# Kernel optimization log

Hardware: AMD Instinct MI355X
Metric: run time of the kernel (lower is better)

The kernel has to match this reference:

```python
import jax, jax.numpy as jnp
import numpy as np

NUM_HEADS = 32
NUM_KV_HEADS = 8
HEAD_DIM = 128
WINDOW = 256
NUM_META = 128
ROPE_BASE = 10000.0


def _rope_cos_sin(seq_len, dim, dtype):
    inv_freq = 1.0 / (ROPE_BASE ** (jnp.arange(0, dim, 2, dtype=jnp.float32) / dim))
    pos = jnp.arange(seq_len, dtype=jnp.float32)
    freqs = pos[:, None] * inv_freq[None, :]          # [S, dim/2]
    emb = jnp.concatenate([freqs, freqs], axis=-1)     # [S, dim]
    return emb.astype(dtype) * 0 + jnp.cos(emb).astype(dtype), jnp.sin(emb).astype(dtype)


def _rotate_half(x):
    x1, x2 = jnp.split(x, 2, axis=-1)
    return jnp.concatenate([-x2, x1], axis=-1)


def setup_inputs() -> dict:
    key = jax.random.key(0)
    k1, k2, k3 = jax.random.split(key, 3)
    B, S = 1, 2176
    return {
        "query_states": jax.random.normal(k1, (B, S, NUM_HEADS * HEAD_DIM), dtype=jnp.float32),
        "key_states": jax.random.normal(k2, (B, S, NUM_KV_HEADS * HEAD_DIM), dtype=jnp.float32),
        "value_states": jax.random.normal(k3, (B, S, NUM_KV_HEADS * HEAD_DIM), dtype=jnp.float32),
    }


def reference(query_states, key_states, value_states):
    B, S, _ = query_states.shape
    n_rep = NUM_HEADS // NUM_KV_HEADS

    q = query_states.reshape(B, S, NUM_HEADS, HEAD_DIM).transpose(0, 2, 1, 3)      # [B,H,S,D]
    k = key_states.reshape(B, S, NUM_KV_HEADS, HEAD_DIM).transpose(0, 2, 1, 3)     # [B,Hk,S,D]
    v = value_states.reshape(B, S, NUM_KV_HEADS, HEAD_DIM).transpose(0, 2, 1, 3)

    # GQA expansion: repeat_interleave along head dim
    k = jnp.repeat(k, n_rep, axis=1)   # [B,H,S,D]
    v = jnp.repeat(v, n_rep, axis=1)

    # inline RoPE on q and (expanded) k
    cos, sin = _rope_cos_sin(S, HEAD_DIM, q.dtype)     # [S,D]
    cos = cos[None, None]
    sin = sin[None, None]
    q = q * cos + _rotate_half(q) * sin
    k = k * cos + _rotate_half(k) * sin

    scale = 1.0 / jnp.sqrt(jnp.asarray(HEAD_DIM, q.dtype))
    scores = jnp.einsum("bhqd,bhkd->bhqk", q, k) * scale

    # mask: causal AND (sliding window OR kv is a prefix meta token)
    q_idx = jnp.arange(S)[:, None]
    kv_idx = jnp.arange(S)[None, :]
    causal = q_idx >= kv_idx
    sliding = (q_idx - kv_idx) <= WINDOW
    prefix = kv_idx < NUM_META
    mask = causal & (sliding | prefix)                 # [S,S]

    scores = jnp.where(mask[None, None], scores, jnp.asarray(-jnp.inf, scores.dtype))
    probs = jax.nn.softmax(scores, axis=-1)
    out = jnp.einsum("bhqk,bhkd->bhqd", probs, v)      # [B,H,S,D]
    return out.transpose(0, 2, 1, 3).reshape(B, S, NUM_HEADS * HEAD_DIM)
```

## Files before the change

kernel.cpp:

```cpp
#include <hip/hip_runtime.h>

#define HQ 32
#define HKV 8
#define DH 128
#define WIN 256
#define META 128
#define QSCALE 0.1275174324f
#define NFREQ 0.20762050594046f

typedef __attribute__((ext_vector_type(8))) __bf16 bf16x8;
typedef __attribute__((ext_vector_type(16))) float f32x16;
typedef __attribute__((ext_vector_type(4))) unsigned int u32x4;
typedef unsigned short u16;
typedef unsigned int u32;

__device__ __forceinline__ u16 f2bf(float f) {
  u32 u = __float_as_uint(f);
  u += 0x7FFFu + ((u >> 16) & 1u);
  return (u16)(u >> 16);
}
__device__ __forceinline__ u32 packbf(float a, float b) {
  u32 ua = __float_as_uint(a); ua += 0x7FFFu + ((ua >> 16) & 1u);
  u32 ub = __float_as_uint(b); ub += 0x7FFFu + ((ub >> 16) & 1u);
  return (ua >> 16) | (ub & 0xFFFF0000u);
}

__global__ __launch_bounds__(256)
void prep_kv(const float* __restrict__ Kg, const float* __restrict__ Vg,
             u16* __restrict__ Kr, u16* __restrict__ Vt, int S) {
  __shared__ float T[64][132];
  const int hk = blockIdx.x;
  const int s0 = blockIdx.y * 64;
  const int tid = threadIdx.x;
  {
    const int r = tid >> 2, c0 = (tid & 3) * 16;
    const int s = s0 + r;
    const float pos = (float)s;
    const float* src = Kg + ((size_t)s * HKV + hk) * DH;
    u16* dst = Kr + ((size_t)hk * S + s) * DH;
    float x[16], y[16];
    #pragma unroll
    for (int j = 0; j < 16; j += 4) {
      *(float4*)&x[j] = *(const float4*)(src + c0 + j);
      *(float4*)&y[j] = *(const float4*)(src + c0 + 64 + j);
    }
    u16 lo[16], hb[16];
    #pragma unroll
    for (int j = 0; j < 16; ++j) {
      float iv = __builtin_amdgcn_exp2f(-NFREQ * (float)(c0 + j));
      float sv, cv; __sincosf(pos * iv, &sv, &cv);
      lo[j] = f2bf(x[j] * cv - y[j] * sv);
      hb[j] = f2bf(y[j] * cv + x[j] * sv);
    }
    *(int4*)(dst + c0)      = *(int4*)&lo[0];
    *(int4*)(dst + c0 + 8)  = *(int4*)&lo[8];
    *(int4*)(dst + c0 + 64) = *(int4*)&hb[0];
    *(int4*)(dst + c0 + 72) = *(int4*)&hb[8];
  }
  {
    const int r = tid >> 2, c = (tid & 3) * 32;
    const float* src = Vg + ((size_t)(s0 + r) * HKV + hk) * DH + c;
    #pragma unroll
    for (int j = 0; j < 32; j += 4) *(float4*)&T[r][c + j] = *(const float4*)(src + j);
  }
  __syncthreads();
  {
    const int d = tid >> 1, hf = (tid & 1) * 32;
    u16 buf[32];
    #pragma unroll
    for (int i = 0; i < 32; ++i) buf[i] = f2bf(T[hf + i][d]);
    u16* dst = Vt + ((size_t)hk * DH + d) * S + s0 + hf;
    #pragma unroll
    for (int j = 0; j < 4; ++j) *(int4*)(dst + j * 8) = *(int4*)&buf[j * 8];
  }
}

__global__ __launch_bounds__(256, 2)
void attn_main(const float* __restrict__ Qg, const u16* __restrict__ Kr,
               const u16* __restrict__ Vt, float* __restrict__ Og, int S) {
  const int h = blockIdx.x;
  const int nqb = gridDim.y;
  const int q0 = (nqb - 1 - blockIdx.y) * 128;
  const int hk = h >> 2;
  const int tid = threadIdx.x;
  const int lane = tid & 63;
  const int wave = tid >> 6;
  const int ln31 = lane & 31;
  const int hi = lane >> 5;
  const int kh = hi * 8;

  __shared__ __align__(16) char smem[35840];
  u16 (*Qs)[136] = (u16(*)[136])smem;
  u16 (*Ks)[136] = (u16(*)[136])smem;
  u16 (*Vs)[72]  = (u16(*)[72])(smem + 17408);

  {
    const int r = tid >> 1, c0 = (tid & 1) * 32;
    const float pos = (float)(q0 + r);
    const float* qrow = Qg + ((size_t)(q0 + r) * HQ + h) * DH;
    #pragma unroll
    for (int c = c0; c < c0 + 32; c += 8) {
      float x[8], y[8];
      *(float4*)&x[0] = *(const float4*)(qrow + c);
      *(float4*)&x[4] = *(const float4*)(qrow + c + 4);
      *(float4*)&y[0] = *(const float4*)(qrow + c + 64);
      *(float4*)&y[4] = *(const float4*)(qrow + c + 68);
      u16 lo[8], hb[8];
      #pragma unroll
      for (int j = 0; j < 8; ++j) {
        float iv = __builtin_amdgcn_exp2f(-NFREQ * (float)(c + j));
        float sv, cv; __sincosf(pos * iv, &sv, &cv);
        lo[j] = f2bf((x[j] * cv - y[j] * sv) * QSCALE);
        hb[j] = f2bf((y[j] * cv + x[j] * sv) * QSCALE);
      }
      __builtin_memcpy(&Qs[r][c], lo, 16);
      __builtin_memcpy(&Qs[r][c + 64], hb, 16);
    }
  }
  __syncthreads();
  const int qw0 = q0 + wave * 32;
  const int q = qw0 + ln31;
  bf16x8 qa[8];
  {
    const u16* qb = &Qs[wave * 32 + ln31][kh];
    #pragma unroll
    for (int kk = 0; kk < 8; ++kk) qa[kk] = *(const bf16x8*)(qb + kk * 16);
  }

  int wstart = q0 - WIN; if (wstart < META) wstart = META;
  int nwin = (q0 + 128 - wstart) >> 6; if (nwin < 0) nwin = 0;
  const int ntiles = 2 + nwin;

  f32x16 acc[4];
  #pragma unroll
  for (int d = 0; d < 4; ++d)
    #pragma unroll
    for (int r = 0; r < 16; ++r) acc[d][r] = 0.f;
  float m_i = -1e30f, l_i = 0.f;

  const u16* Kb = Kr + (size_t)hk * S * DH;
  const u16* Vb = Vt + ((size_t)hk * DH + (tid >> 1)) * S + (tid & 1) * 32;
  const int kr = tid >> 2, kc = (tid & 3) * 32;

  for (int t = 0; t < ntiles; ++t) {
    const int kv0 = (t < 2) ? t * 64 : wstart + (t - 2) * 64;

    __syncthreads();
    {
      const int4* ks = (const int4*)(Kb + (size_t)(kv0 + kr) * DH + kc);
      int4 a = ks[0], b = ks[1], c = ks[2], d = ks[3];
      int4* kd = (int4*)&Ks[kr][kc];
      kd[0] = a; kd[1] = b; kd[2] = c; kd[3] = d;
    }
    {
      const int4* vs = (const int4*)(Vb + kv0);
      int4 a = vs[0], b = vs[1], c = vs[2], d = vs[3];
      int4* vd = (int4*)&Vs[tid >> 1][(tid & 1) * 32];
      vd[0] = a; vd[1] = b; vd[2] = c; vd[3] = d;
    }
    __syncthreads();

    const bool active = (kv0 <= qw0 + 31) &&
                        ((kv0 < META) || (qw0 - kv0 - 63 <= WIN));
    if (!active) continue;

    f32x16 s0v, s1v;
    #pragma unroll
    for (int r = 0; r < 16; ++r) { s0v[r] = 0.f; s1v[r] = 0.f; }
    const u16* ka0 = &Ks[ln31][kh];
    const u16* ka1 = &Ks[32 + ln31][kh];
    #pragma unroll
    for (int kk = 0; kk < 8; ++kk)
      s0v = __builtin_amdgcn_mfma_f32_32x32x16_bf16(*(const bf16x8*)(ka0 + kk * 16), qa[kk], s0v, 0, 0, 0);
    #pragma unroll
    for (int kk = 0; kk < 8; ++kk)
      s1v = __builtin_amdgcn_mfma_f32_32x32x16_bf16(*(const bf16x8*)(ka1 + kk * 16), qa[kk], s1v, 0, 0, 0);

    const bool fullv = (kv0 + 63 <= qw0) &&
                       ((kv0 + 63 < META) || (qw0 + 31 - kv0 <= WIN));
    if (!fullv) {
      #pragma unroll
      for (int r = 0; r < 16; ++r) {
        const int kva = kv0 + (r & 3) + 8 * (r >> 2) + 4 * hi;
        const int kvb = kva + 32;
        if (!((kva <= q) && (((q - kva) <= WIN) || (kva < META)))) s0v[r] = -1e30f;
        if (!((kvb <= q) && (((q - kvb) <= WIN) || (kvb < META)))) s1v[r] = -1e30f;
      }
    }

    float mx = -1e30f;
    #pragma unroll
    for (int r = 0; r < 16; ++r) mx = fmaxf(mx, fmaxf(s0v[r], s1v[r]));
    mx = fmaxf(mx, __shfl_xor(mx, 32));
    const float mnew = fmaxf(m_i, mx);
    const float al = __builtin_amdgcn_exp2f(m_i - mnew);
    m_i = mnew;
    float ps = 0.f;
    #pragma unroll
    for (int r = 0; r < 16; ++r) {
      s0v[r] = __builtin_amdgcn_exp2f(s0v[r] - mnew);
      s1v[r] = __builtin_amdgcn_exp2f(s1v[r] - mnew);
      ps += s0v[r] + s1v[r];
    }
    ps += __shfl_xor(ps, 32);
    l_i = l_i * al + ps;
    #pragma unroll
    for (int d = 0; d < 4; ++d)
      #pragma unroll
      for (int r = 0; r < 16; ++r) acc[d][r] *= al;

    u32 pk0[8], pk1[8], sh0[8], sh1[8];
    #pragma unroll
    for (int m = 0; m < 8; ++m) {
      pk0[m] = packbf(s0v[2 * m], s0v[2 * m + 1]);
      pk1[m] = packbf(s1v[2 * m], s1v[2 * m + 1]);
    }
    #pragma unroll
    for (int m = 0; m < 8; ++m) {
      sh0[m] = (u32)__shfl_xor((int)pk0[m], 32);
      sh1[m] = (u32)__shfl_xor((int)pk1[m], 32);
    }
    u32x4 bl0 = { hi ? sh0[2] : pk0[0], hi ? sh0[3] : pk0[1],
                  hi ? pk0[2] : sh0[0], hi ? pk0[3] : sh0[1] };
    u32x4 bh0 = { hi ? sh0[6] : pk0[4], hi ? sh0[7] : pk0[5],
                  hi ? pk0[6] : sh0[4], hi ? pk0[7] : sh0[5] };
    u32x4 bl1 = { hi ? sh1[2] : pk1[0], hi ? sh1[3] : pk1[1],
                  hi ? pk1[2] : sh1[0], hi ? pk1[3] : sh1[1] };
    u32x4 bh1 = { hi ? sh1[6] : pk1[4], hi ? sh1[7] : pk1[5],
                  hi ? pk1[6] : sh1[4], hi ? pk1[7] : sh1[5] };
    const bf16x8 pbl0 = __builtin_bit_cast(bf16x8, bl0);
    const bf16x8 pbh0 = __builtin_bit_cast(bf16x8, bh0);
    const bf16x8 pbl1 = __builtin_bit_cast(bf16x8, bl1);
    const bf16x8 pbh1 = __builtin_bit_cast(bf16x8, bh1);

    #pragma unroll
    for (int dt = 0; dt < 4; ++dt) {
      const u16* vrow = &Vs[dt * 32 + ln31][kh];
      acc[dt] = __builtin_amdgcn_mfma_f32_32x32x16_bf16(*(const bf16x8*)(vrow),      pbl0, acc[dt], 0, 0, 0);
      acc[dt] = __builtin_amdgcn_mfma_f32_32x32x16_bf16(*(const bf16x8*)(vrow + 16), pbh0, acc[dt], 0, 0, 0);
      acc[dt] = __builtin_amdgcn_mfma_f32_32x32x16_bf16(*(const bf16x8*)(vrow + 32), pbl1, acc[dt], 0, 0, 0);
      acc[dt] = __builtin_amdgcn_mfma_f32_32x32x16_bf16(*(const bf16x8*)(vrow + 48), pbh1, acc[dt], 0, 0, 0);
    }
  }

  const float inv = 1.0f / l_i;
  float* ob = Og + ((size_t)q * HQ + h) * DH;
  #pragma unroll
  for (int dt = 0; dt < 4; ++dt) {
    #pragma unroll
    for (int g = 0; g < 4; ++g) {
      float4 o = { acc[dt][4 * g + 0] * inv, acc[dt][4 * g + 1] * inv,
                   acc[dt][4 * g + 2] * inv, acc[dt][4 * g + 3] * inv };
      *(float4*)(ob + dt * 32 + 8 * g + 4 * hi) = o;
    }
  }
}

extern "C" void kernel_launch(void* const* d_in, const int* in_sizes, int n_in,
                              void* d_out, int out_size, void* d_ws, size_t ws_size,
                              hipStream_t stream) {
  const float* Qg = (const float*)d_in[0];
  const float* Kg = (const float*)d_in[1];
  const float* Vg = (const float*)d_in[2];
  float* Og = (float*)d_out;
  const int S = in_sizes[0] / (HQ * DH);

  u16* Kr = (u16*)d_ws;
  u16* Vt = (u16*)((char*)d_ws + (size_t)HKV * S * DH * 2);

  prep_kv<<<dim3(HKV, S / 64), dim3(256), 0, stream>>>(Kg, Vg, Kr, Vt, S);
  attn_main<<<dim3(HQ, S / 128), dim3(256), 0, stream>>>(Qg, Kr, Vt, Og, S);
}
```

Before: 136.3 us.

## Prefetch next K/V tile into registers while computing current tile

Global loads for the next K/V tile are issued into registers before the current tile's QK, softmax and PV work, and written to shared memory after it. The first tile's load is issued before the Q RoPE prologue. This is meant to hide global memory latency behind MFMA work. The cost is 32 more live VGPRs per thread under the 2-blocks-per-SM launch bound, which could cause spills or lower occupancy.

After: 133.3 us. 1.02x faster.

```diff
diff --git a/kernel.cpp b/kernel.cpp
--- a/kernel.cpp
+++ b/kernel.cpp
@@ -74,6 +74,20 @@
     for (int j = 0; j < 4; ++j) *(int4*)(dst + j * 8) = *(int4*)&buf[j * 8];
   }
 }
+
+#define LOAD_KV(kv0_) do {                                                 \
+    const int4* ks_ = (const int4*)(Kb + (size_t)((kv0_) + kr) * DH + kc); \
+    fk0 = ks_[0]; fk1 = ks_[1]; fk2 = ks_[2]; fk3 = ks_[3];                \
+    const int4* vs_ = (const int4*)(Vb + (kv0_));                          \
+    fv0 = vs_[0]; fv1 = vs_[1]; fv2 = vs_[2]; fv3 = vs_[3];                \
+  } while (0)
+
+#define STORE_KV() do {                                                    \
+    int4* kd_ = (int4*)&Ks[kr][kc];                                        \
+    kd_[0] = fk0; kd_[1] = fk1; kd_[2] = fk2; kd_[3] = fk3;                \
+    int4* vd_ = (int4*)&Vs[tid >> 1][(tid & 1) * 32];                      \
+    vd_[0] = fv0; vd_[1] = fv1; vd_[2] = fv2; vd_[3] = fv3;                \
+  } while (0)
 
 __global__ __launch_bounds__(256, 2)
 void attn_main(const float* __restrict__ Qg, const u16* __restrict__ Kr,
@@ -94,6 +108,13 @@
   u16 (*Ks)[136] = (u16(*)[136])smem;
   u16 (*Vs)[72]  = (u16(*)[72])(smem + 17408);
 
+  const u16* Kb = Kr + (size_t)hk * S * DH;
+  const u16* Vb = Vt + ((size_t)hk * DH + (tid >> 1)) * S + (tid & 1) * 32;
+  const int kr = tid >> 2, kc = (tid & 3) * 32;
+
+  int4 fk0, fk1, fk2, fk3, fv0, fv1, fv2, fv3;
+  LOAD_KV(0);
+
   {
     const int r = tid >> 1, c0 = (tid & 1) * 32;
     const float pos = (float)(q0 + r);
@@ -126,6 +147,9 @@
     #pragma unroll
     for (int kk = 0; kk < 8; ++kk) qa[kk] = *(const bf16x8*)(qb + kk * 16);
   }
+  __syncthreads();
+  STORE_KV();
+  __syncthreads();
 
   int wstart = q0 - WIN; if (wstart < META) wstart = META;
   int nwin = (q0 + 128 - wstart) >> 6; if (nwin < 0) nwin = 0;
@@ -138,108 +162,100 @@
     for (int r = 0; r < 16; ++r) acc[d][r] = 0.f;
   float m_i = -1e30f, l_i = 0.f;
 
-  const u16* Kb = Kr + (size_t)hk * S * DH;
-  const u16* Vb = Vt + ((size_t)hk * DH + (tid >> 1)) * S + (tid & 1) * 32;
-  const int kr = tid >> 2, kc = (tid & 3) * 32;
-
   for (int t = 0; t < ntiles; ++t) {
     const int kv0 = (t < 2) ? t * 64 : wstart + (t - 2) * 64;
-
-    __syncthreads();
-    {
-      const int4* ks = (const int4*)(Kb + (size_t)(kv0 + kr) * DH + kc);
-      int4 a = ks[0], b = ks[1], c = ks[2], d = ks[3];
-      int4* kd = (int4*)&Ks[kr][kc];
-      kd[0] = a; kd[1] = b; kd[2] = c; kd[3] = d;
-    }
-    {
-      const int4* vs = (const int4*)(Vb + kv0);
-      int4 a = vs[0], b = vs[1], c = vs[2], d = vs[3];
-      int4* vd = (int4*)&Vs[tid >> 1][(tid & 1) * 32];
-      vd[0] = a; vd[1] = b; vd[2] = c; vd[3] = d;
-    }
-    __syncthreads();
+    const bool haveNext = (t + 1 < ntiles);
+    if (haveNext) {
+      const int kvn = (t + 1 < 2) ? (t + 1) * 64 : wstart + (t - 1) * 64;
+      LOAD_KV(kvn);
+    }
 
     const bool active = (kv0 <= qw0 + 31) &&
                         ((kv0 < META) || (qw0 - kv0 - 63 <= WIN));
-    if (!active) continue;
-
-    f32x16 s0v, s1v;
-    #pragma unroll
-    for (int r = 0; r < 16; ++r) { s0v[r] = 0.f; s1v[r] = 0.f; }
-    const u16* ka0 = &Ks[ln31][kh];
-    const u16* ka1 = &Ks[32 + ln31][kh];
-    #pragma unroll
-    for (int kk = 0; kk < 8; ++kk)
-      s0v = __builtin_amdgcn_mfma_f32_32x32x16_bf16(*(const bf16x8*)(ka0 + kk * 16), qa[kk], s0v, 0, 0, 0);
-    #pragma unroll
-    for (int kk = 0; kk < 8; ++kk)
-      s1v = __builtin_amdgcn_mfma_f32_32x32x16_bf16(*(const bf16x8*)(ka1 + kk * 16), qa[kk], s1v, 0, 0, 0);
-
-    const bool fullv = (kv0 + 63 <= qw0) &&
-                       ((kv0 + 63 < META) || (qw0 + 31 - kv0 <= WIN));
-    if (!fullv) {
+    if (active) {
+      f32x16 s0v, s1v;
+      #pragma unroll
+      for (int r = 0; r < 16; ++r) { s0v[r] = 0.f; s1v[r] = 0.f; }
+      const u16* ka0 = &Ks[ln31][kh];
+      const u16* ka1 = &Ks[32 + ln31][kh];
+      #pragma unroll
+      for (int kk = 0; kk < 8; ++kk)
+        s0v = __builtin_amdgcn_mfma_f32_32x32x16_bf16(*(const bf16x8*)(ka0 + kk * 16), qa[kk], s0v, 0, 0, 0);
+      #pragma unroll
+      for (int kk = 0; kk < 8; ++kk)
+        s1v = __builtin_amdgcn_mfma_f32_32x32x16_bf16(*(const bf16x8*)(ka1 + kk * 16), qa[kk], s1v, 0, 0, 0);
+
+      const bool fullv = (kv0 + 63 <= qw0) &&
+                         ((kv0 + 63 < META) || (qw0 + 31 - kv0 <= WIN));
+      if (!fullv) {
+        #pragma unroll
+        for (int r = 0; r < 16; ++r) {
+          const int kva = kv0 + (r & 3) + 8 * (r >> 2) + 4 * hi;
+          const int kvb = kva + 32;
+          if (!((kva <= q) && (((q - kva) <= WIN) || (kva < META)))) s0v[r] = -1e30f;
+          if (!((kvb <= q) && (((q - kvb) <= WIN) || (kvb < META)))) s1v[r] = -1e30f;
+        }
+      }
+
+      float mx = -1e30f;
+      #pragma unroll
+      for (int r = 0; r < 16; ++r) mx = fmaxf(mx, fmaxf(s0v[r], s1v[r]));
+      mx = fmaxf(mx, __shfl_xor(mx, 32));
+      const float mnew = fmaxf(m_i, mx);
+      const float al = __builtin_amdgcn_exp2f(m_i - mnew);
+      m_i = mnew;
+      float ps = 0.f;
       #pragma unroll
       for (int r = 0; r < 16; ++r) {
-        const int kva = kv0 + (r & 3) + 8 * (r >> 2) + 4 * hi;
-        const int kvb = kva + 32;
-        if (!((kva <= q) && (((q - kva) <= WIN) || (kva < META)))) s0v[r] = -1e30f;
-        if (!((kvb <= q) && (((q - kvb) <= WIN) || (kvb < META)))) s1v[r] = -1e30f;
-      }
-    }
-
-    float mx = -1e30f;
-    #pragma unroll
-    for (int r = 0; r < 16; ++r) mx = fmaxf(mx, fmaxf(s0v[r], s1v[r]));
-    mx = fmaxf(mx, __shfl_xor(mx, 32));
-    const float mnew = fmaxf(m_i, mx);
-    const float al = __builtin_amdgcn_exp2f(m_i - mnew);
-    m_i = mnew;
-    float ps = 0.f;
-    #pragma unroll
-    for (int r = 0; r < 16; ++r) {
-      s0v[r] = __builtin_amdgcn_exp2f(s0v[r] - mnew);
-      s1v[r] = __builtin_amdgcn_exp2f(s1v[r] - mnew);
-      ps += s0v[r] + s1v[r];
-    }
-    ps += __shfl_xor(ps, 32);
-    l_i = l_i * al + ps;
-    #pragma unroll
-    for (int d = 0; d < 4; ++d)
-      #pragma unroll
-      for (int r = 0; r < 16; ++r) acc[d][r] *= al;
-
-    u32 pk0[8], pk1[8], sh0[8], sh1[8];
-    #pragma unroll
-    for (int m = 0; m < 8; ++m) {
-      pk0[m] = packbf(s0v[2 * m], s0v[2 * m + 1]);
-      pk1[m] = packbf(s1v[2 * m], s1v[2 * m + 1]);
-    }
-    #pragma unroll
-    for (int m = 0; m < 8; ++m) {
-      sh0[m] = (u32)__shfl_xor((int)pk0[m], 32);
-      sh1[m] = (u32)__shfl_xor((int)pk1[m], 32);
-    }
-    u32x4 bl0 = { hi ? sh0[2] : pk0[0], hi ? sh0[3] : pk0[1],
-                  hi ? pk0[2] : sh0[0], hi ? pk0[3] : sh0[1] };
-    u32x4 bh0 = { hi ? sh0[6] : pk0[4], hi ? sh0[7] : pk0[5],
-                  hi ? pk0[6] : sh0[4], hi ? pk0[7] : sh0[5] };
-    u32x4 bl1 = { hi ? sh1[2] : pk1[0], hi ? sh1[3] : pk1[1],
-                  hi ? pk1[2] : sh1[0], hi ? pk1[3] : sh1[1] };
-    u32x4 bh1 = { hi ? sh1[6] : pk1[4], hi ? sh1[7] : pk1[5],
-                  hi ? pk1[6] : sh1[4], hi ? pk1[7] : sh1[5] };
-    const bf16x8 pbl0 = __builtin_bit_cast(bf16x8, bl0);
-    const bf16x8 pbh0 = __builtin_bit_cast(bf16x8, bh0);
-    const bf16x8 pbl1 = __builtin_bit_cast(bf16x8, bl1);
-    const bf16x8 pbh1 = __builtin_bit_cast(bf16x8, bh1);
-
-    #pragma unroll
-    for (int dt = 0; dt < 4; ++dt) {
-      const u16* vrow = &Vs[dt * 32 + ln31][kh];
-      acc[dt] = __builtin_amdgcn_mfma_f32_32x32x16_bf16(*(const bf16x8*)(vrow),      pbl0, acc[dt], 0, 0, 0);
-      acc[dt] = __builtin_amdgcn_mfma_f32_32x32x16_bf16(*(const bf16x8*)(vrow + 16), pbh0, acc[dt], 0, 0, 0);
-      acc[dt] = __builtin_amdgcn_mfma_f32_32x32x16_bf16(*(const bf16x8*)(vrow + 32), pbl1, acc[dt], 0, 0, 0);
-      acc[dt] = __builtin_amdgcn_mfma_f32_32x32x16_bf16(*(const bf16x8*)(vrow + 48), pbh1, acc[dt], 0, 0, 0);
+        s0v[r] = __builtin_amdgcn_exp2f(s0v[r] - mnew);
+        s1v[r] = __builtin_amdgcn_exp2f(s1v[r] - mnew);
+        ps += s0v[r] + s1v[r];
+      }
+      ps += __shfl_xor(ps, 32);
+      l_i = l_i * al + ps;
+      #pragma unroll
+      for (int d = 0; d < 4; ++d)
+        #pragma unroll
+        for (int r = 0; r < 16; ++r) acc[d][r] *= al;
+
+      u32 pk0[8], pk1[8], sh0[8], sh1[8];
+      #pragma unroll
+      for (int m = 0; m < 8; ++m) {
+        pk0[m] = packbf(s0v[2 * m], s0v[2 * m + 1]);
+        pk1[m] = packbf(s1v[2 * m], s1v[2 * m + 1]);
+      }
+      #pragma unroll
+      for (int m = 0; m < 8; ++m) {
+        sh0[m] = (u32)__shfl_xor((int)pk0[m], 32);
+        sh1[m] = (u32)__shfl_xor((int)pk1[m], 32);
+      }
+      u32x4 bl0 = { hi ? sh0[2] : pk0[0], hi ? sh0[3] : pk0[1],
+                    hi ? pk0[2] : sh0[0], hi ? pk0[3] : sh0[1] };
+      u32x4 bh0 = { hi ? sh0[6] : pk0[4], hi ? sh0[7] : pk0[5],
+                    hi ? pk0[6] : sh0[4], hi ? pk0[7] : sh0[5] };
+      u32x4 bl1 = { hi ? sh1[2] : pk1[0], hi ? sh1[3] : pk1[1],
+                    hi ? pk1[2] : sh1[0], hi ? pk1[3] : sh1[1] };
+      u32x4 bh1 = { hi ? sh1[6] : pk1[4], hi ? sh1[7] : pk1[5],
+                    hi ? pk1[6] : sh1[4], hi ? pk1[7] : sh1[5] };
+      const bf16x8 pbl0 = __builtin_bit_cast(bf16x8, bl0);
+      const bf16x8 pbh0 = __builtin_bit_cast(bf16x8, bh0);
+      const bf16x8 pbl1 = __builtin_bit_cast(bf16x8, bl1);
+      const bf16x8 pbh1 = __builtin_bit_cast(bf16x8, bh1);
+
+      #pragma unroll
+      for (int dt = 0; dt < 4; ++dt) {
+        const u16* vrow = &Vs[dt * 32 + ln31][kh];
+        acc[dt] = __builtin_amdgcn_mfma_f32_32x32x16_bf16(*(const bf16x8*)(vrow),      pbl0, acc[dt], 0, 0, 0);
+        acc[dt] = __builtin_amdgcn_mfma_f32_32x32x16_bf16(*(const bf16x8*)(vrow + 16), pbh0, acc[dt], 0, 0, 0);
+        acc[dt] = __builtin_amdgcn_mfma_f32_32x32x16_bf16(*(const bf16x8*)(vrow + 32), pbl1, acc[dt], 0, 0, 0);
+        acc[dt] = __builtin_amdgcn_mfma_f32_32x32x16_bf16(*(const bf16x8*)(vrow + 48), pbh1, acc[dt], 0, 0, 0);
+      }
+    }
+
+    if (haveNext) {
+      __syncthreads();
+      STORE_KV();
+      __syncthreads();
     }
   }
 
```
